# Performance work log

Measured on AMD Instinct MI355X. Metric: run time of the kernel, lower is better.

## Reference

```python
import jax, jax.numpy as jnp
import numpy as np

NUM_GRAPHS = 64


def gcn_conv(x, src, dst, num_nodes, W, b):
    # PyG GCNConv: linear first, then normalized aggregation, bias after.
    h = x @ W  # [N, out]
    # degree with self-loops already included in (src, dst)
    deg = jax.ops.segment_sum(jnp.ones_like(src, dtype=h.dtype), dst, num_segments=num_nodes)
    dinv = jnp.where(deg > 0, jax.lax.rsqrt(jnp.maximum(deg, 1e-12)), 0.0)
    norm = dinv[src] * dinv[dst]  # [E]
    msg = h[src] * norm[:, None]  # [E, out] gather + scale
    out = jax.ops.segment_sum(msg, dst, num_segments=num_nodes)  # scatter-add
    return out + b


def setup_inputs() -> dict:
    key = jax.random.key(0)
    ks = jax.random.split(key, 12)
    N, E = 50000, 400000
    dims = [36, 75, 150, 50]
    x = jax.random.normal(ks[0], (N, dims[0]), dtype=jnp.float32)
    edge_index = jax.random.randint(ks[1], (2, E), 0, N, dtype=jnp.int64)
    batch = jnp.sort(jax.random.randint(ks[2], (N,), 0, NUM_GRAPHS, dtype=jnp.int64))
    def glorot(k, fi, fo):
        lim = np.sqrt(6.0 / (fi + fo)).astype(np.float32)
        return jax.random.uniform(k, (fi, fo), jnp.float32, -lim, lim)
    inp = {"x": x, "edge_index": edge_index, "batch": batch}
    for i in range(3):
        inp[f"W{i+1}"] = glorot(ks[3 + 2 * i], dims[i], dims[i + 1])
        inp[f"b{i+1}"] = jnp.zeros((dims[i + 1],), jnp.float32)
    inp["Wo"] = glorot(ks[9], dims[3], 3)
    inp["bo"] = jnp.zeros((3,), jnp.float32)
    return inp


def reference(x, edge_index, batch, W1, b1, W2, b2, W3, b3, Wo, bo):
    N = x.shape[0]
    loop = jnp.arange(N, dtype=edge_index.dtype)
    src = jnp.concatenate([edge_index[0], loop])  # add self-loops
    dst = jnp.concatenate([edge_index[1], loop])
    h = x
    for W, b in ((W1, b1), (W2, b2), (W3, b3)):
        h = gcn_conv(h, src, dst, N, W, b)
        h = jax.nn.relu(h)  # dropout is identity in eval mode
    h = h @ Wo + bo  # [N, 3]
    pooled = jax.ops.segment_max(h, batch, num_segments=NUM_GRAPHS)  # [G, 3]
    return jax.nn.softmax(pooled, axis=1)
```

## Files before the change

kernel.cpp:

```cpp
#include <hip/hip_runtime.h>
#include <hip/hip_bf16.h>

#define DIV_UP(a, b) (((a) + (b) - 1) / (b))
typedef long long ll;
typedef __attribute__((ext_vector_type(8))) short short8;
typedef __attribute__((ext_vector_type(4))) float f32x4;

__device__ __forceinline__ float ldf(const void* p, ll i, int bf) {
    return bf ? __bfloat162float(((const __hip_bfloat16*)p)[i]) : ((const float*)p)[i];
}
__device__ __forceinline__ int ldi(const int* p, ll i, int w) {
    return w ? p[2 * i] : p[i];
}
template <int MODE>
__device__ __forceinline__ float ldm(const void* p, ll i, int bf) {
    if (MODE == 1) return __bfloat162float(((const __hip_bfloat16*)p)[i]);
    return ldf(p, i, bf);
}

__device__ __forceinline__ unsigned fenc(float f) {
    unsigned u = __float_as_uint(f);
    return (u & 0x80000000u) ? ~u : (u | 0x80000000u);
}
__device__ __forceinline__ float fdec(unsigned u) {
    unsigned v = (u & 0x80000000u) ? (u & 0x7FFFFFFFu) : ~u;
    return __uint_as_float(v);
}
#define ENC_NEG_INF 0x007FFFFFu

#define MB1 0
#define MB2 80
#define MHW 240
#define MB3 390
#define MBO 440
#define N_MISC 444
#define P1 0
#define P2 5120
#define P3 20480
#define N_PACK 30720

__global__ void k_detect(const unsigned* __restrict__ xb, const unsigned* __restrict__ eb,
                         int* __restrict__ flags) {
    __shared__ int sv[2];
    int t = threadIdx.x;
    if (t < 2) sv[t] = 0;
    __syncthreads();
    unsigned e = (xb[t] >> 7) & 0xFFu;
    int vote = (e >= 115u && e <= 133u) ? 1 : 0;
    int zero = (eb[2 * t + 1] == 0u) ? 1 : 0;
    atomicAdd(&sv[0], vote);
    atomicAdd(&sv[1], zero);
    __syncthreads();
    if (t == 0) {
        flags[0] = (sv[0] > 128) ? 1 : 0;
        flags[1] = (sv[1] > 200) ? 1 : 0;
    }
}

__global__ void k_cvt_misc(const void* __restrict__ b1, const void* __restrict__ b2,
                           const void* __restrict__ Wo, const void* __restrict__ b3,
                           const void* __restrict__ bo, float* __restrict__ wfm,
                           const int* __restrict__ flags) {
    int t = blockIdx.x * blockDim.x + threadIdx.x;
    if (t >= N_MISC) return;
    int bf = flags[0];
    float v = 0.0f;
    if (t < 75)
        v = ldf(b1, t, bf);
    else if (t >= MB2 && t < MB2 + 150)
        v = ldf(b2, t - MB2, bf);
    else if (t >= MHW && t < MHW + 150)
        v = ldf(Wo, t - MHW, bf);
    else if (t >= MB3 && t < MB3 + 50)
        v = ldf(b3, t - MB3, bf);
    else if (t >= MBO && t < MBO + 3)
        v = ldf(bo, t - MBO, bf);
    wfm[t] = v;
}

__global__ void k_cvt_pack(const void* __restrict__ W1, const void* __restrict__ W2,
                           const void* __restrict__ W3, __hip_bfloat16* __restrict__ wp,
                           const int* __restrict__ flags) {
    int t = blockIdx.x * blockDim.x + threadIdx.x;
    if (t >= N_PACK) return;
    int bf = flags[0];
    const void* W;
    int i, K, OUT, KC;
    if (t < P2) {
        W = W1;
        i = t;
        K = 36;
        OUT = 75;
        KC = 2;
    } else if (t < P3) {
        W = W2;
        i = t - P2;
        K = 75;
        OUT = 150;
        KC = 3;
    } else {
        W = W3;
        i = t - P3;
        K = 150;
        OUT = 50;
        KC = 5;
    }
    int j = i & 7;
    int lane = (i >> 3) & 63;
    int tile = i >> 9;
    int kc = tile % KC;
    int ct = tile / KC;
    int k = kc * 32 + ((lane >> 4) << 3) + j;
    int col = ct * 16 + (lane & 15);
    float v = (k < K && col < OUT) ? ldf(W, (ll)k * OUT + col, bf) : 0.0f;
    wp[t] = __float2bfloat16(v);
}

__global__ void k_zero(int* p, int n) {
    int t = blockIdx.x * blockDim.x + threadIdx.x;
    if (t < n) p[t] = 0;
}
__global__ void k_hist(const int* __restrict__ ei, int* __restrict__ cnt,
                       const int* __restrict__ flags, int E) {
    int t = blockIdx.x * blockDim.x + threadIdx.x;
    if (t >= E) return;
    atomicAdd(&cnt[ldi(ei, (ll)E + t, flags[1])], 1);
}
__global__ void k_scan1(const int* __restrict__ cnt, int* __restrict__ bsum,
                        float* __restrict__ dinv, int N) {
    __shared__ int s[256];
    int t = threadIdx.x;
    int idx = blockIdx.x * 256 + t;
    int v = (idx < N) ? cnt[idx] : 0;
    if (idx < N) dinv[idx] = rsqrtf((float)v + 1.0f);
    s[t] = v;
    __syncthreads();
#pragma unroll
    for (int off = 128; off > 0; off >>= 1) {
        if (t < off) s[t] += s[t + off];
        __syncthreads();
    }
    if (t == 0) bsum[blockIdx.x] = s[0];
}
__global__ void k_scan2(int* __restrict__ bsum, int nb) {
    __shared__ int s[256];
    int t = threadIdx.x;
    int run = 0;
    for (int base = 0; base < nb; base += 256) {
        int i = base + t;
        int v = (i < nb) ? bsum[i] : 0;
        s[t] = v;
        __syncthreads();
        for (int off = 1; off < 256; off <<= 1) {
            int o = (t >= off) ? s[t - off] : 0;
            __syncthreads();
            s[t] += o;
            __syncthreads();
        }
        if (i < nb) bsum[i] = run + s[t] - v;
        run += s[255];
        __syncthreads();
    }
}
__global__ void k_scan3(const int* __restrict__ cnt, const int* __restrict__ bsum,
                        int* __restrict__ rowptr, int N) {
    __shared__ int s[256];
    int t = threadIdx.x;
    int idx = blockIdx.x * 256 + t;
    int v = (idx < N) ? cnt[idx] : 0;
    s[t] = v;
    __syncthreads();
    for (int off = 1; off < 256; off <<= 1) {
        int o = (t >= off) ? s[t - off] : 0;
        __syncthreads();
        s[t] += o;
        __syncthreads();
    }
    if (idx <= N) rowptr[idx] = bsum[blockIdx.x] + s[t] - v;
}
__global__ void k_fill(const int* __restrict__ ei, const int* __restrict__ rowptr,
                       int* __restrict__ cursor, int2* __restrict__ ep,
                       const float* __restrict__ dinv, const int* __restrict__ flags, int E) {
    int t = blockIdx.x * blockDim.x + threadIdx.x;
    if (t >= E) return;
    int wi = flags[1];
    int s = ldi(ei, t, wi);
    int d = ldi(ei, (ll)E + t, wi);
    int pos = rowptr[d] + atomicAdd(&cursor[d], 1);
    int2 v;
    v.x = s;
    v.y = __float_as_int(dinv[s] * dinv[d]);
    ep[pos] = v;
}

template <int MODE, int OD>
__global__ void k_agg(const void* __restrict__ X, int xstride, void* __restrict__ Yv, int ystride,
                      int C, const int* __restrict__ rowptr, const int2* __restrict__ ep,
                      const float* __restrict__ dinv, const int* __restrict__ flags, int N) {
    int n = blockIdx.x * 4 + (threadIdx.x >> 6);
    if (n >= N) return;
    int lane = threadIdx.x & 63;
    int bf = (MODE == 2) ? flags[0] : 0;
    float di = dinv[n];
    float w0 = di * di;
    int c1 = lane + 64;
    bool has0 = lane < C, has1 = c1 < C;
    float a0 = has0 ? w0 * ldm<MODE>(X, (ll)n * xstride + lane, bf) : 0.0f;
    float a1 = has1 ? w0 * ldm<MODE>(X, (ll)n * xstride + c1, bf) : 0.0f;
    int j = rowptr[n];
    int je = rowptr[n + 1];
    for (; j + 3 < je; j += 4) {
        int2 v0 = ep[j];
        int2 v1 = ep[j + 1];
        int2 v2 = ep[j + 2];
        int2 v3 = ep[j + 3];
        float wa = __int_as_float(v0.y), wb = __int_as_float(v1.y);
        float wc = __int_as_float(v2.y), wd = __int_as_float(v3.y);
        if (has0) {
            a0 = fmaf(wa, ldm<MODE>(X, (ll)v0.x * xstride + lane, bf), a0);
            a0 = fmaf(wb, ldm<MODE>(X, (ll)v1.x * xstride + lane, bf), a0);
            a0 = fmaf(wc, ldm<MODE>(X, (ll)v2.x * xstride + lane, bf), a0);
            a0 = fmaf(wd, ldm<MODE>(X, (ll)v3.x * xstride + lane, bf), a0);
        }
        if (has1) {
            a1 = fmaf(wa, ldm<MODE>(X, (ll)v0.x * xstride + c1, bf), a1);
            a1 = fmaf(wb, ldm<MODE>(X, (ll)v1.x * xstride + c1, bf), a1);
            a1 = fmaf(wc, ldm<MODE>(X, (ll)v2.x * xstride + c1, bf), a1);
            a1 = fmaf(wd, ldm<MODE>(X, (ll)v3.x * xstride + c1, bf), a1);
        }
    }
    for (; j < je; ++j) {
        int2 v0 = ep[j];
        float wa = __int_as_float(v0.y);
        if (has0) a0 = fmaf(wa, ldm<MODE>(X, (ll)v0.x * xstride + lane, bf), a0);
        if (has1) a1 = fmaf(wa, ldm<MODE>(X, (ll)v0.x * xstride + c1, bf), a1);
    }
    if (has0) {
        if (OD)
            ((__hip_bfloat16*)Yv)[(ll)n * ystride + lane] = __float2bfloat16(a0);
        else
            ((float*)Yv)[(ll)n * ystride + lane] = a0;
    }
    if (has1) {
        if (OD)
            ((__hip_bfloat16*)Yv)[(ll)n * ystride + c1] = __float2bfloat16(a1);
        else
            ((float*)Yv)[(ll)n * ystride + c1] = a1;
    }
}

template <int K, int KC, int OUT, int CT, bool RELU, bool BIAS>
__global__ __launch_bounds__(256) void k_gemm(const __hip_bfloat16* __restrict__ X, int xs,
                                              __hip_bfloat16* __restrict__ Y, int ys,
                                              const short8* __restrict__ Wp,
                                              const float* __restrict__ bias, int N) {
    const int lane = threadIdx.x & 63;
    const int wid = threadIdx.x >> 6;
    const int m0 = blockIdx.x * 64 + wid * 16;
    const int mrow = lane & 15;
    const int koct = lane >> 4;
    const __hip_bfloat16* xrow = X + (ll)(m0 + mrow) * xs + koct * 8;
    f32x4 acc[CT];
#pragma unroll
    for (int ct = 0; ct < CT; ++ct)
#pragma unroll
        for (int r = 0; r < 4; ++r) acc[ct][r] = 0.0f;
    float bv[CT];
#pragma unroll
    for (int ct = 0; ct < CT; ++ct) {
        int col = ct * 16 + mrow;
        bv[ct] = (BIAS && col < OUT) ? bias[col] : 0.0f;
    }
#pragma unroll 1
    for (int kc = 0; kc < KC; ++kc) {
        short8 a = *(const short8*)(xrow + kc * 32);
#pragma unroll
        for (int ct = 0; ct < CT; ++ct) {
            short8 b = Wp[(ct * KC + kc) * 64 + lane];
            acc[ct] = __builtin_amdgcn_mfma_f32_16x16x32_bf16(a, b, acc[ct], 0, 0, 0);
        }
    }
#pragma unroll
    for (int ct = 0; ct < CT; ++ct) {
        int col = ct * 16 + mrow;
        if (col >= OUT) continue;
#pragma unroll
        for (int r = 0; r < 4; ++r) {
            int node = m0 + koct * 4 + r;
            if (node >= N) continue;
            float v = acc[ct][r] + bv[ct];
            if (RELU) v = fmaxf(v, 0.0f);
            Y[(ll)node * ys + col] = __float2bfloat16(v);
        }
    }
}

__global__ void k_pool_init(unsigned* pooled) {
    int t = threadIdx.x;
    if (t < 64 * 3) pooled[t] = ENC_NEG_INF;
}

__global__ void k_head(const float* __restrict__ Y3, int ystride, const float* __restrict__ wfm,
                       const int* __restrict__ batch, unsigned* __restrict__ pooled,
                       const int* __restrict__ flags, int N) {
    __shared__ float Ws[50 * 3];
    __shared__ float bs[50];
    __shared__ float bos[3];
    __shared__ unsigned lmax[192];
    int wi = flags[1];
    for (int i = threadIdx.x; i < 150; i += blockDim.x) Ws[i] = wfm[MHW + i];
    for (int i = threadIdx.x; i < 50; i += blockDim.x) bs[i] = wfm[MB3 + i];
    if (threadIdx.x < 3) bos[threadIdx.x] = wfm[MBO + threadIdx.x];
    for (int i = threadIdx.x; i < 192; i += blockDim.x) lmax[i] = ENC_NEG_INF;
    __syncthreads();
    int n = blockIdx.x * blockDim.x + threadIdx.x;
    int lane = threadIdx.x & 63;
    float z0 = 0.0f, z1 = 0.0f, z2 = 0.0f;
    int g = 0;
    if (n < N) {
        z0 = bos[0];
        z1 = bos[1];
        z2 = bos[2];
        const float* y = Y3 + (ll)n * ystride;
#pragma unroll
        for (int k = 0; k < 50; ++k) {
            float h = fmaxf(y[k] + bs[k], 0.0f);
            z0 = fmaf(h, Ws[k * 3 + 0], z0);
            z1 = fmaf(h, Ws[k * 3 + 1], z1);
            z2 = fmaf(h, Ws[k * 3 + 2], z2);
        }
        g = ldi(batch, n, wi);
    }
    int g0 = __shfl(g, 0);
    unsigned long long uni = __ballot(n < N && g == g0);
    if (uni == ~0ULL) {
#pragma unroll
        for (int off = 32; off > 0; off >>= 1) {
            z0 = fmaxf(z0, __shfl_xor(z0, off));
            z1 = fmaxf(z1, __shfl_xor(z1, off));
            z2 = fmaxf(z2, __shfl_xor(z2, off));
        }
        if (lane == 0) {
            atomicMax(&lmax[g0 * 3 + 0], fenc(z0));
            atomicMax(&lmax[g0 * 3 + 1], fenc(z1));
            atomicMax(&lmax[g0 * 3 + 2], fenc(z2));
        }
    } else if (n < N) {
        atomicMax(&lmax[g * 3 + 0], fenc(z0));
        atomicMax(&lmax[g * 3 + 1], fenc(z1));
        atomicMax(&lmax[g * 3 + 2], fenc(z2));
    }
    __syncthreads();
    for (int i = threadIdx.x; i < 192; i += blockDim.x) {
        unsigned v = lmax[i];
        if (v != ENC_NEG_INF) atomicMax(&pooled[i], v);
    }
}

__global__ void k_softmax(const unsigned* __restrict__ pooled, void* __restrict__ out,
                          const int* __restrict__ flags) {
    int g = threadIdx.x;
    if (g >= 64) return;
    int bf = flags[0];
    float a = fdec(pooled[g * 3 + 0]);
    float b = fdec(pooled[g * 3 + 1]);
    float c = fdec(pooled[g * 3 + 2]);
    float m = fmaxf(a, fmaxf(b, c));
    float ea = __expf(a - m), eb = __expf(b - m), ec = __expf(c - m);
    float s = 1.0f / (ea + eb + ec);
    if (bf) {
        __hip_bfloat16* o = (__hip_bfloat16*)out;
        o[g * 3 + 0] = __float2bfloat16(ea * s);
        o[g * 3 + 1] = __float2bfloat16(eb * s);
        o[g * 3 + 2] = __float2bfloat16(ec * s);
    } else {
        float* o = (float*)out;
        o[g * 3 + 0] = ea * s;
        o[g * 3 + 1] = eb * s;
        o[g * 3 + 2] = ec * s;
    }
}

extern "C" void kernel_launch(void* const* d_in, const int* in_sizes, int n_in,
                              void* d_out, int out_size, void* d_ws, size_t ws_size,
                              hipStream_t stream) {
    const void* x = d_in[0];
    const int* ei = (const int*)d_in[1];
    const int* batch = (const int*)d_in[2];

    const int N = in_sizes[0] / 36;
    const int E = in_sizes[1] / 2;

    char* ws = (char*)d_ws;
    size_t off = 0;
    auto carve = [&](size_t bytes) {
        char* p = ws + off;
        off = (off + bytes + 255) & ~(size_t)255;
        return p;
    };
    int* flags = (int*)carve(16);
    float* wfm = (float*)carve((size_t)N_MISC * 4);
    __hip_bfloat16* wpack = (__hip_bfloat16*)carve((size_t)N_PACK * 2);
    float* dinv = (float*)carve((size_t)N * 4);
    int* cnt = (int*)carve((size_t)N * 4);
    int* rowptr = (int*)carve((size_t)(N + 1) * 4);
    int2* ep = (int2*)carve((size_t)E * 8);
    unsigned* pooled = (unsigned*)carve(768);
    const int NB = DIV_UP(N + 1, 256);
    int* bsum = (int*)carve((size_t)NB * 4);
    char* R1 = carve((size_t)N * 192);
    char* R2 = carve((size_t)N * 320);
    (void)carve(65536);

    const int B = 256;
    const int GB = DIV_UP(N, 64);

    k_detect<<<1, 256, 0, stream>>>((const unsigned*)x, (const unsigned*)ei, flags);
    k_cvt_misc<<<2, 256, 0, stream>>>(d_in[4], d_in[6], d_in[9], d_in[8], d_in[10], wfm, flags);
    k_cvt_pack<<<DIV_UP(N_PACK, B), B, 0, stream>>>(d_in[3], d_in[5], d_in[7], wpack, flags);

    k_zero<<<DIV_UP(N, B), B, 0, stream>>>(cnt, N);
    k_hist<<<DIV_UP(E, B), B, 0, stream>>>(ei, cnt, flags, E);
    k_scan1<<<NB, 256, 0, stream>>>(cnt, bsum, dinv, N);
    k_scan2<<<1, 256, 0, stream>>>(bsum, NB);
    k_scan3<<<NB, 256, 0, stream>>>(cnt, bsum, rowptr, N);
    k_zero<<<DIV_UP(N, B), B, 0, stream>>>(cnt, N);
    k_fill<<<DIV_UP(E, B), B, 0, stream>>>(ei, rowptr, cnt, ep, dinv, flags, E);

    k_agg<2, 1><<<DIV_UP(N, 4), B, 0, stream>>>(x, 36, R1, 64, 36, rowptr, ep, dinv, flags, N);
    k_gemm<36, 2, 75, 5, true, true><<<GB, B, 0, stream>>>(
        (const __hip_bfloat16*)R1, 64, (__hip_bfloat16*)R2, 80, (const short8*)(wpack + P1),
        wfm + MB1, N);

    k_agg<1, 1><<<DIV_UP(N, 4), B, 0, stream>>>(R2, 80, R1, 96, 75, rowptr, ep, dinv, flags, N);
    k_gemm<75, 3, 150, 10, true, true><<<GB, B, 0, stream>>>(
        (const __hip_bfloat16*)R1, 96, (__hip_bfloat16*)R2, 160, (const short8*)(wpack + P2),
        wfm + MB2, N);

    k_gemm<150, 5, 50, 4, false, false><<<GB, B, 0, stream>>>(
        (const __hip_bfloat16*)R2, 160, (__hip_bfloat16*)R1, 64, (const short8*)(wpack + P3), wfm,
        N);
    k_agg<1, 0><<<DIV_UP(N, 4), B, 0, stream>>>(R1, 64, R2, 50, 50, rowptr, ep, dinv, flags, N);

    k_pool_init<<<1, 192, 0, stream>>>(pooled);
    k_head<<<DIV_UP(N, B), B, 0, stream>>>((const float*)R2, 50, wfm, batch, pooled, flags, N);
    k_softmax<<<1, 64, 0, stream>>>(pooled, d_out, flags);
}
```

Baseline: 281.6 us.

## Fuse small setup kernels, pack bf16 pairs in aggregation, fuse layer-3 head

Several tiny setup kernels are merged: zeroing the counts moves into k_detect and k_scan3, pool init moves into k_scan2, and the two weight-conversion kernels become one. Layers 2 and 3 aggregation now read two bf16 channels per lane through 32-bit loads. The final aggregation also applies bias, ReLU and the 50x3 output projection with a warp reduction, so a smaller [N,3] buffer goes to a lighter pooling kernel. The aim is fewer launches and fewer gather transactions. The cost is that the layer-3 output projection now runs through a warp shuffle reduction for every node.

```diff
diff --git a/kernel.cpp b/kernel.cpp
--- a/kernel.cpp
+++ b/kernel.cpp
@@ -16,6 +16,10 @@
 __device__ __forceinline__ float ldm(const void* p, ll i, int bf) {
     if (MODE == 1) return __bfloat162float(((const __hip_bfloat16*)p)[i]);
     return ldf(p, i, bf);
+}
+__device__ __forceinline__ void bf16pair(unsigned u, float& f0, float& f1) {
+    f0 = __uint_as_float(u << 16);
+    f1 = __uint_as_float(u & 0xFFFF0000u);
 }
 
 __device__ __forceinline__ unsigned fenc(float f) {
@@ -40,7 +44,10 @@
 #define N_PACK 30720
 
 __global__ void k_detect(const unsigned* __restrict__ xb, const unsigned* __restrict__ eb,
-                         int* __restrict__ flags) {
+                         int* __restrict__ flags, int* __restrict__ cnt, int N) {
+    int idx = blockIdx.x * 256 + threadIdx.x;
+    if (idx < N) cnt[idx] = 0;
+    if (blockIdx.x != 0) return;
     __shared__ int sv[2];
     int t = threadIdx.x;
     if (t < 2) sv[t] = 0;
@@ -57,69 +64,63 @@
     }
 }
 
-__global__ void k_cvt_misc(const void* __restrict__ b1, const void* __restrict__ b2,
-                           const void* __restrict__ Wo, const void* __restrict__ b3,
-                           const void* __restrict__ bo, float* __restrict__ wfm,
-                           const int* __restrict__ flags) {
+__global__ void k_cvt(const void* __restrict__ W1, const void* __restrict__ b1,
+                      const void* __restrict__ W2, const void* __restrict__ b2,
+                      const void* __restrict__ W3, const void* __restrict__ b3,
+                      const void* __restrict__ Wo, const void* __restrict__ bo,
+                      __hip_bfloat16* __restrict__ wp, float* __restrict__ wfm,
+                      const int* __restrict__ flags) {
     int t = blockIdx.x * blockDim.x + threadIdx.x;
-    if (t >= N_MISC) return;
     int bf = flags[0];
-    float v = 0.0f;
-    if (t < 75)
-        v = ldf(b1, t, bf);
-    else if (t >= MB2 && t < MB2 + 150)
-        v = ldf(b2, t - MB2, bf);
-    else if (t >= MHW && t < MHW + 150)
-        v = ldf(Wo, t - MHW, bf);
-    else if (t >= MB3 && t < MB3 + 50)
-        v = ldf(b3, t - MB3, bf);
-    else if (t >= MBO && t < MBO + 3)
-        v = ldf(bo, t - MBO, bf);
-    wfm[t] = v;
-}
-
-__global__ void k_cvt_pack(const void* __restrict__ W1, const void* __restrict__ W2,
-                           const void* __restrict__ W3, __hip_bfloat16* __restrict__ wp,
-                           const int* __restrict__ flags) {
-    int t = blockIdx.x * blockDim.x + threadIdx.x;
-    if (t >= N_PACK) return;
-    int bf = flags[0];
-    const void* W;
-    int i, K, OUT, KC;
-    if (t < P2) {
-        W = W1;
-        i = t;
-        K = 36;
-        OUT = 75;
-        KC = 2;
-    } else if (t < P3) {
-        W = W2;
-        i = t - P2;
-        K = 75;
-        OUT = 150;
-        KC = 3;
+    if (t < N_PACK) {
+        const void* W;
+        int i, K, OUT, KC;
+        if (t < P2) {
+            W = W1;
+            i = t;
+            K = 36;
+            OUT = 75;
+            KC = 2;
+        } else if (t < P3) {
+            W = W2;
+            i = t - P2;
+            K = 75;
+            OUT = 150;
+            KC = 3;
+        } else {
+            W = W3;
+            i = t - P3;
+            K = 150;
+            OUT = 50;
+            KC = 5;
+        }
+        int j = i & 7;
+        int lane = (i >> 3) & 63;
+        int tile = i >> 9;
+        int kc = tile % KC;
+        int ct = tile / KC;
+        int k = kc * 32 + ((lane >> 4) << 3) + j;
+        int col = ct * 16 + (lane & 15);
+        float v = (k < K && col < OUT) ? ldf(W, (ll)k * OUT + col, bf) : 0.0f;
+        wp[t] = __float2bfloat16(v);
     } else {
-        W = W3;
-        i = t - P3;
-        K = 150;
-        OUT = 50;
-        KC = 5;
-    }
-    int j = i & 7;
-    int lane = (i >> 3) & 63;
-    int tile = i >> 9;
-    int kc = tile % KC;
-    int ct = tile / KC;
-    int k = kc * 32 + ((lane >> 4) << 3) + j;
-    int col = ct * 16 + (lane & 15);
-    float v = (k < K && col < OUT) ? ldf(W, (ll)k * OUT + col, bf) : 0.0f;
-    wp[t] = __float2bfloat16(v);
-}
-
-__global__ void k_zero(int* p, int n) {
-    int t = blockIdx.x * blockDim.x + threadIdx.x;
-    if (t < n) p[t] = 0;
-}
+        int m = t - N_PACK;
+        if (m >= N_MISC) return;
+        float v = 0.0f;
+        if (m < 75)
+            v = ldf(b1, m, bf);
+        else if (m >= MB2 && m < MB2 + 150)
+            v = ldf(b2, m - MB2, bf);
+        else if (m >= MHW && m < MHW + 150)
+            v = ldf(Wo, m - MHW, bf);
+        else if (m >= MB3 && m < MB3 + 50)
+            v = ldf(b3, m - MB3, bf);
+        else if (m >= MBO && m < MBO + 3)
+            v = ldf(bo, m - MBO, bf);
+        wfm[m] = v;
+    }
+}
+
 __global__ void k_hist(const int* __restrict__ ei, int* __restrict__ cnt,
                        const int* __restrict__ flags, int E) {
     int t = blockIdx.x * blockDim.x + threadIdx.x;
@@ -142,9 +143,10 @@
     }
     if (t == 0) bsum[blockIdx.x] = s[0];
 }
-__global__ void k_scan2(int* __restrict__ bsum, int nb) {
+__global__ void k_scan2(int* __restrict__ bsum, int nb, unsigned* __restrict__ pooled) {
     __shared__ int s[256];
     int t = threadIdx.x;
+    if (t < 192) pooled[t] = ENC_NEG_INF;
     int run = 0;
     for (int base = 0; base < nb; base += 256) {
         int i = base + t;
@@ -162,12 +164,13 @@
         __syncthreads();
     }
 }
-__global__ void k_scan3(const int* __restrict__ cnt, const int* __restrict__ bsum,
+__global__ void k_scan3(int* __restrict__ cnt, const int* __restrict__ bsum,
                         int* __restrict__ rowptr, int N) {
     __shared__ int s[256];
     int t = threadIdx.x;
     int idx = blockIdx.x * 256 + t;
     int v = (idx < N) ? cnt[idx] : 0;
+    if (idx < N) cnt[idx] = 0;
     s[t] = v;
     __syncthreads();
     for (int off = 1; off < 256; off <<= 1) {
@@ -193,20 +196,18 @@
     ep[pos] = v;
 }
 
-template <int MODE, int OD>
-__global__ void k_agg(const void* __restrict__ X, int xstride, void* __restrict__ Yv, int ystride,
-                      int C, const int* __restrict__ rowptr, const int2* __restrict__ ep,
-                      const float* __restrict__ dinv, const int* __restrict__ flags, int N) {
+__global__ void k_agg(const void* __restrict__ X, int xstride, __hip_bfloat16* __restrict__ Y,
+                      int ystride, int C, const int* __restrict__ rowptr,
+                      const int2* __restrict__ ep, const float* __restrict__ dinv,
+                      const int* __restrict__ flags, int N) {
     int n = blockIdx.x * 4 + (threadIdx.x >> 6);
     if (n >= N) return;
     int lane = threadIdx.x & 63;
-    int bf = (MODE == 2) ? flags[0] : 0;
+    int bf = flags[0];
     float di = dinv[n];
     float w0 = di * di;
-    int c1 = lane + 64;
-    bool has0 = lane < C, has1 = c1 < C;
-    float a0 = has0 ? w0 * ldm<MODE>(X, (ll)n * xstride + lane, bf) : 0.0f;
-    float a1 = has1 ? w0 * ldm<MODE>(X, (ll)n * xstride + c1, bf) : 0.0f;
+    if (lane >= C) return;
+    float a0 = w0 * ldm<2>(X, (ll)n * xstride + lane, bf);
     int j = rowptr[n];
     int je = rowptr[n + 1];
     for (; j + 3 < je; j += 4) {
@@ -214,38 +215,166 @@
         int2 v1 = ep[j + 1];
         int2 v2 = ep[j + 2];
         int2 v3 = ep[j + 3];
-        float wa = __int_as_float(v0.y), wb = __int_as_float(v1.y);
-        float wc = __int_as_float(v2.y), wd = __int_as_float(v3.y);
-        if (has0) {
-            a0 = fmaf(wa, ldm<MODE>(X, (ll)v0.x * xstride + lane, bf), a0);
-            a0 = fmaf(wb, ldm<MODE>(X, (ll)v1.x * xstride + lane, bf), a0);
-            a0 = fmaf(wc, ldm<MODE>(X, (ll)v2.x * xstride + lane, bf), a0);
-            a0 = fmaf(wd, ldm<MODE>(X, (ll)v3.x * xstride + lane, bf), a0);
-        }
-        if (has1) {
-            a1 = fmaf(wa, ldm<MODE>(X, (ll)v0.x * xstride + c1, bf), a1);
-            a1 = fmaf(wb, ldm<MODE>(X, (ll)v1.x * xstride + c1, bf), a1);
-            a1 = fmaf(wc, ldm<MODE>(X, (ll)v2.x * xstride + c1, bf), a1);
-            a1 = fmaf(wd, ldm<MODE>(X, (ll)v3.x * xstride + c1, bf), a1);
-        }
+        a0 = fmaf(__int_as_float(v0.y), ldm<2>(X, (ll)v0.x * xstride + lane, bf), a0);
+        a0 = fmaf(__int_as_float(v1.y), ldm<2>(X, (ll)v1.x * xstride + lane, bf), a0);
+        a0 = fmaf(__int_as_float(v2.y), ldm<2>(X, (ll)v2.x * xstride + lane, bf), a0);
+        a0 = fmaf(__int_as_float(v3.y), ldm<2>(X, (ll)v3.x * xstride + lane, bf), a0);
     }
     for (; j < je; ++j) {
         int2 v0 = ep[j];
+        a0 = fmaf(__int_as_float(v0.y), ldm<2>(X, (ll)v0.x * xstride + lane, bf), a0);
+    }
+    Y[(ll)n * ystride + lane] = __float2bfloat16(a0);
+}
+
+__global__ void k_aggp(const __hip_bfloat16* __restrict__ X, int xs,
+                       __hip_bfloat16* __restrict__ Y, int ys, int CP,
+                       const int* __restrict__ rowptr, const int2* __restrict__ ep,
+                       const float* __restrict__ dinv, int N) {
+    int n = blockIdx.x * 4 + (threadIdx.x >> 6);
+    if (n >= N) return;
+    int lane = threadIdx.x & 63;
+    if (lane >= CP) return;
+    float di = dinv[n];
+    float w0 = di * di;
+    float a0, a1;
+    {
+        unsigned u = *(const unsigned*)(X + (ll)n * xs + 2 * lane);
+        float f0, f1;
+        bf16pair(u, f0, f1);
+        a0 = w0 * f0;
+        a1 = w0 * f1;
+    }
+    int j = rowptr[n];
+    int je = rowptr[n + 1];
+    for (; j + 3 < je; j += 4) {
+        int2 v0 = ep[j];
+        int2 v1 = ep[j + 1];
+        int2 v2 = ep[j + 2];
+        int2 v3 = ep[j + 3];
+        unsigned u0 = *(const unsigned*)(X + (ll)v0.x * xs + 2 * lane);
+        unsigned u1 = *(const unsigned*)(X + (ll)v1.x * xs + 2 * lane);
+        unsigned u2 = *(const unsigned*)(X + (ll)v2.x * xs + 2 * lane);
+        unsigned u3 = *(const unsigned*)(X + (ll)v3.x * xs + 2 * lane);
+        float f0, f1;
+        bf16pair(u0, f0, f1);
         float wa = __int_as_float(v0.y);
-        if (has0) a0 = fmaf(wa, ldm<MODE>(X, (ll)v0.x * xstride + lane, bf), a0);
-        if (has1) a1 = fmaf(wa, ldm<MODE>(X, (ll)v0.x * xstride + c1, bf), a1);
-    }
-    if (has0) {
-        if (OD)
-            ((__hip_bfloat16*)Yv)[(ll)n * ystride + lane] = __float2bfloat16(a0);
-        else
-            ((float*)Yv)[(ll)n * ystride + lane] = a0;
-    }
-    if (has1) {
-        if (OD)
-            ((__hip_bfloat16*)Yv)[(ll)n * ystride + c1] = __float2bfloat16(a1);
-        else
-            ((float*)Yv)[(ll)n * ystride + c1] = a1;
+        a0 = fmaf(wa, f0, a0);
+        a1 = fmaf(wa, f1, a1);
+        bf16pair(u1, f0, f1);
+        wa = __int_as_float(v1.y);
+        a0 = fmaf(wa, f0, a0);
+        a1 = fmaf(wa, f1, a1);
+        bf16pair(u2, f0, f1);
+        wa = __int_as_float(v2.y);
+        a0 = fmaf(wa, f0, a0);
+        a1 = fmaf(wa, f1, a1);
+        bf16pair(u3, f0, f1);
+        wa = __int_as_float(v3.y);
+        a0 = fmaf(wa, f0, a0);
+        a1 = fmaf(wa, f1, a1);
+    }
+    for (; j < je; ++j) {
+        int2 v0 = ep[j];
+        unsigned u = *(const unsigned*)(X + (ll)v0.x * xs + 2 * lane);
+        float f0, f1;
+        bf16pair(u, f0, f1);
+        float wa = __int_as_float(v0.y);
+        a0 = fmaf(wa, f0, a0);
+        a1 = fmaf(wa, f1, a1);
+    }
+    __hip_bfloat162 h;
+    h.x = __float2bfloat16(a0);
+    h.y = __float2bfloat16(a1);
+    *(__hip_bfloat162*)(Y + (ll)n * ys + 2 * lane) = h;
+}
+
+__global__ void k_agg3h(const __hip_bfloat16* __restrict__ X, int xs, float* __restrict__ zb,
+                        const int* __restrict__ rowptr, const int2* __restrict__ ep,
+                        const float* __restrict__ dinv, const float* __restrict__ wfm, int N) {
+    int n = blockIdx.x * 4 + (threadIdx.x >> 6);
+    if (n >= N) return;
+    int lane = threadIdx.x & 63;
+    bool act = lane < 25;
+    int c0 = 2 * lane;
+    float w00 = 0, w01 = 0, w02 = 0, w10 = 0, w11 = 0, w12 = 0, bb0 = 0, bb1 = 0;
+    if (act) {
+        w00 = wfm[MHW + c0 * 3 + 0];
+        w01 = wfm[MHW + c0 * 3 + 1];
+        w02 = wfm[MHW + c0 * 3 + 2];
+        w10 = wfm[MHW + c0 * 3 + 3];
+        w11 = wfm[MHW + c0 * 3 + 4];
+        w12 = wfm[MHW + c0 * 3 + 5];
+        bb0 = wfm[MB3 + c0];
+        bb1 = wfm[MB3 + c0 + 1];
+    }
+    float di = dinv[n];
+    float w0 = di * di;
+    float a0 = 0.0f, a1 = 0.0f;
+    if (act) {
+        unsigned u = *(const unsigned*)(X + (ll)n * xs + 2 * lane);
+        float f0, f1;
+        bf16pair(u, f0, f1);
+        a0 = w0 * f0;
+        a1 = w0 * f1;
+    }
+    int j = rowptr[n];
+    int je = rowptr[n + 1];
+    for (; j + 3 < je; j += 4) {
+        int2 v0 = ep[j];
+        int2 v1 = ep[j + 1];
+        int2 v2 = ep[j + 2];
+        int2 v3 = ep[j + 3];
+        if (act) {
+            unsigned u0 = *(const unsigned*)(X + (ll)v0.x * xs + 2 * lane);
+            unsigned u1 = *(const unsigned*)(X + (ll)v1.x * xs + 2 * lane);
+            unsigned u2 = *(const unsigned*)(X + (ll)v2.x * xs + 2 * lane);
+            unsigned u3 = *(const unsigned*)(X + (ll)v3.x * xs + 2 * lane);
+            float f0, f1;
+            bf16pair(u0, f0, f1);
+            float wa = __int_as_float(v0.y);
+            a0 = fmaf(wa, f0, a0);
+            a1 = fmaf(wa, f1, a1);
+            bf16pair(u1, f0, f1);
+            wa = __int_as_float(v1.y);
+            a0 = fmaf(wa, f0, a0);
+            a1 = fmaf(wa, f1, a1);
+            bf16pair(u2, f0, f1);
+            wa = __int_as_float(v2.y);
+            a0 = fmaf(wa, f0, a0);
+            a1 = fmaf(wa, f1, a1);
+            bf16pair(u3, f0, f1);
+            wa = __int_as_float(v3.y);
+            a0 = fmaf(wa, f0, a0);
+            a1 = fmaf(wa, f1, a1);
+        }
+    }
+    for (; j < je; ++j) {
+        int2 v0 = ep[j];
+        if (act) {
+            unsigned u = *(const unsigned*)(X + (ll)v0.x * xs + 2 * lane);
+            float f0, f1;
+            bf16pair(u, f0, f1);
+            float wa = __int_as_float(v0.y);
+            a0 = fmaf(wa, f0, a0);
+            a1 = fmaf(wa, f1, a1);
+        }
+    }
+    float h0 = act ? fmaxf(a0 + bb0, 0.0f) : 0.0f;
+    float h1 = act ? fmaxf(a1 + bb1, 0.0f) : 0.0f;
+    float z0 = h0 * w00 + h1 * w10;
+    float z1 = h0 * w01 + h1 * w11;
+    float z2 = h0 * w02 + h1 * w12;
+#pragma unroll
+    for (int off = 32; off > 0; off >>= 1) {
+        z0 += __shfl_xor(z0, off);
+        z1 += __shfl_xor(z1, off);
+        z2 += __shfl_xor(z2, off);
+    }
+    if (lane == 0) {
+        zb[(ll)n * 3 + 0] = z0 + wfm[MBO + 0];
+        zb[(ll)n * 3 + 1] = z1 + wfm[MBO + 1];
+        zb[(ll)n * 3 + 2] = z2 + wfm[MBO + 2];
     }
 }
 
@@ -295,40 +424,20 @@
     }
 }
 
-__global__ void k_pool_init(unsigned* pooled) {
-    int t = threadIdx.x;
-    if (t < 64 * 3) pooled[t] = ENC_NEG_INF;
-}
-
-__global__ void k_head(const float* __restrict__ Y3, int ystride, const float* __restrict__ wfm,
-                       const int* __restrict__ batch, unsigned* __restrict__ pooled,
-                       const int* __restrict__ flags, int N) {
-    __shared__ float Ws[50 * 3];
-    __shared__ float bs[50];
-    __shared__ float bos[3];
+__global__ void k_pool(const float* __restrict__ zb, const int* __restrict__ batch,
+                       unsigned* __restrict__ pooled, const int* __restrict__ flags, int N) {
     __shared__ unsigned lmax[192];
     int wi = flags[1];
-    for (int i = threadIdx.x; i < 150; i += blockDim.x) Ws[i] = wfm[MHW + i];
-    for (int i = threadIdx.x; i < 50; i += blockDim.x) bs[i] = wfm[MB3 + i];
-    if (threadIdx.x < 3) bos[threadIdx.x] = wfm[MBO + threadIdx.x];
     for (int i = threadIdx.x; i < 192; i += blockDim.x) lmax[i] = ENC_NEG_INF;
     __syncthreads();
     int n = blockIdx.x * blockDim.x + threadIdx.x;
     int lane = threadIdx.x & 63;
-    float z0 = 0.0f, z1 = 0.0f, z2 = 0.0f;
+    float z0 = -3.4e38f, z1 = -3.4e38f, z2 = -3.4e38f;
     int g = 0;
     if (n < N) {
-        z0 = bos[0];
-        z1 = bos[1];
-        z2 = bos[2];
-        const float* y = Y3 + (ll)n * ystride;
-#pragma unroll
-        for (int k = 0; k < 50; ++k) {
-            float h = fmaxf(y[k] + bs[k], 0.0f);
-            z0 = fmaf(h, Ws[k * 3 + 0], z0);
-            z1 = fmaf(h, Ws[k * 3 + 1], z1);
-            z2 = fmaf(h, Ws[k * 3 + 2], z2);
-        }
+        z0 = zb[(ll)n * 3 + 0];
+        z1 = zb[(ll)n * 3 + 1];
+        z2 = zb[(ll)n * 3 + 2];
         g = ldi(batch, n, wi);
     }
     int g0 = __shfl(g, 0);
@@ -408,6 +517,7 @@
     unsigned* pooled = (unsigned*)carve(768);
     const int NB = DIV_UP(N + 1, 256);
     int* bsum = (int*)carve((size_t)NB * 4);
+    float* zbuf = (float*)carve((size_t)N * 12);
     char* R1 = carve((size_t)N * 192);
     char* R2 = carve((size_t)N * 320);
     (void)carve(65536);
@@ -415,24 +525,26 @@
     const int B = 256;
     const int GB = DIV_UP(N, 64);
 
-    k_detect<<<1, 256, 0, stream>>>((const unsigned*)x, (const unsigned*)ei, flags);
-    k_cvt_misc<<<2, 256, 0, stream>>>(d_in[4], d_in[6], d_in[9], d_in[8], d_in[10], wfm, flags);
-    k_cvt_pack<<<DIV_UP(N_PACK, B), B, 0, stream>>>(d_in[3], d_in[5], d_in[7], wpack, flags);
-
-    k_zero<<<DIV_UP(N, B), B, 0, stream>>>(cnt, N);
+    k_detect<<<DIV_UP(N, B), B, 0, stream>>>((const unsigned*)x, (const unsigned*)ei, flags, cnt,
+                                             N);
+    k_cvt<<<DIV_UP(N_PACK + N_MISC, B), B, 0, stream>>>(d_in[3], d_in[4], d_in[5], d_in[6],
+                                                        d_in[7], d_in[8], d_in[9], d_in[10], wpack,
+                                                        wfm, flags);
+
     k_hist<<<DIV_UP(E, B), B, 0, stream>>>(ei, cnt, flags, E);
     k_scan1<<<NB, 256, 0, stream>>>(cnt, bsum, dinv, N);
-    k_scan2<<<1, 256, 0, stream>>>(bsum, NB);
+    k_scan2<<<1, 256, 0, stream>>>(bsum, NB, pooled);
     k_scan3<<<NB, 256, 0, stream>>>(cnt, bsum, rowptr, N);
-    k_zero<<<DIV_UP(N, B), B, 0, stream>>>(cnt, N);
     k_fill<<<DIV_UP(E, B), B, 0, stream>>>(ei, rowptr, cnt, ep, dinv, flags, E);
 
-    k_agg<2, 1><<<DIV_UP(N, 4), B, 0, stream>>>(x, 36, R1, 64, 36, rowptr, ep, dinv, flags, N);
+    k_agg<<<DIV_UP(N, 4), B, 0, stream>>>(x, 36, (__hip_bfloat16*)R1, 64, 36, rowptr, ep, dinv,
+                                          flags, N);
     k_gemm<36, 2, 75, 5, true, true><<<GB, B, 0, stream>>>(
         (const __hip_bfloat16*)R1, 64, (__hip_bfloat16*)R2, 80, (const short8*)(wpack + P1),
         wfm + MB1, N);
 
-    k_agg<1, 1><<<DIV_UP(N, 4), B, 0, stream>>>(R2, 80, R1, 96, 75, rowptr, ep, dinv, flags, N);
+    k_aggp<<<DIV_UP(N, 4), B, 0, stream>>>((const __hip_bfloat16*)R2, 80, (__hip_bfloat16*)R1, 96,
+                                           38, rowptr, ep, dinv, N);
     k_gemm<75, 3, 150, 10, true, true><<<GB, B, 0, stream>>>(
         (const __hip_bfloat16*)R1, 96, (__hip_bfloat16*)R2, 160, (const short8*)(wpack + P2),
         wfm + MB2, N);
@@ -440,9 +552,9 @@
     k_gemm<150, 5, 50, 4, false, false><<<GB, B, 0, stream>>>(
         (const __hip_bfloat16*)R2, 160, (__hip_bfloat16*)R1, 64, (const short8*)(wpack + P3), wfm,
         N);
-    k_agg<1, 0><<<DIV_UP(N, 4), B, 0, stream>>>(R1, 64, R2, 50, 50, rowptr, ep, dinv, flags, N);
-
-    k_pool_init<<<1, 192, 0, stream>>>(pooled);
-    k_head<<<DIV_UP(N, B), B, 0, stream>>>((const float*)R2, 50, wfm, batch, pooled, flags, N);
+    k_agg3h<<<DIV_UP(N, 4), B, 0, stream>>>((const __hip_bfloat16*)R1, 64, zbuf, rowptr, ep, dinv,
+                                            wfm, N);
+
+    k_pool<<<DIV_UP(N, B), B, 0, stream>>>(zbuf, batch, pooled, flags, N);
     k_softmax<<<1, 64, 0, stream>>>(pooled, d_out, flags);
 }
```

New measurement: 254.8 us. 9.5% less time.
